# Performance work log

Hardware: AMD Instinct MI355X
Metric: run time of the kernel (lower is better)

The kernel has to match this reference:

```python
import jax, jax.numpy as jnp
import numpy as np

B, N, IN, OUT, H = 16, 1024, 512, 512, 4

def setup_inputs() -> dict:
    key = jax.random.key(0)
    ks = jax.random.split(key, 10)
    s = 0.03  # small init scale to keep tanh/sigmoid in sane range
    return {
        "h": jax.random.normal(ks[0], (B, N, IN), jnp.float32),
        "adj": jax.random.randint(ks[1], (B, N, N), 0, 2) > 0,
        "W": jax.random.normal(ks[2], (H, OUT, IN), jnp.float32) * s,   # per-head Linear weight [out,in]
        "bW": jax.random.normal(ks[3], (H, OUT), jnp.float32) * s,
        "attn": jax.random.normal(ks[4], (H, OUT, OUT), jnp.float32) * s,
        "A_w": jax.random.normal(ks[5], (OUT, OUT * H), jnp.float32) * s,
        "fc_w": jax.random.normal(ks[6], (OUT, IN), jnp.float32) * s,
        "g1_w": jax.random.normal(ks[7], (OUT, OUT), jnp.float32) * s,
        "g2_w": jax.random.normal(ks[8], (OUT, OUT), jnp.float32) * s,
        "gbias": jax.random.normal(ks[9], (OUT,), jnp.float32) * s,
    }

def reference(h, adj, W, bW, attn, A_w, fc_w, g1_w, g2_w, gbias):
    # Per-head projection: Wh[b,h,n,o] = h @ W_h^T + b_h  (dropout is identity at inference)
    Wh = jnp.einsum('bni,hoi->bhno', h, W) + bW[None, :, None, :]
    # Bilinear attention scores: Wh @ attn_h @ Wh^T, masked by adjacency, then tanh
    e = jnp.einsum('bhno,hop->bhnp', Wh, attn)          # [B,H,N,O]
    scores = jnp.einsum('bhnp,bhmp->bhnm', e, Wh)       # [B,H,N,N]
    A_mat = jnp.tanh(jnp.where(adj[:, None, :, :], scores, 0.0))
    # Aggregate neighbors and relu
    hp = jax.nn.relu(jnp.einsum('bhnm,bhmo->bhno', A_mat, Wh))  # [B,H,N,O]
    # Concat heads (relu of relu is identity), project with A
    cat = jnp.transpose(hp, (0, 2, 1, 3)).reshape(hp.shape[0], hp.shape[2], -1)  # [B,N,H*O]
    ha = cat @ A_w.T                                     # [B,N,O]
    hf = h @ fc_w.T                                      # [B,N,O]
    # Sigmoid-gated fusion of the two branches
    coeff = jax.nn.sigmoid(hf @ g1_w.T + ha @ g2_w.T + gbias)
    return hf * coeff + ha * (1.0 - coeff)
```

## Files before the change

### kernel.cpp

```cpp
#include <hip/hip_runtime.h>
#include <hip/hip_fp16.h>


typedef _Float16 h8 __attribute__((ext_vector_type(8)));
typedef _Float16 h4 __attribute__((ext_vector_type(4)));
typedef float f4 __attribute__((ext_vector_type(4)));

__device__ __forceinline__ void load_lds16(const void* g, void* l) {
  __builtin_amdgcn_global_load_lds(
      (const __attribute__((address_space(1))) unsigned int*)g,
      (__attribute__((address_space(3))) unsigned int*)l, 16, 0, 0);
}

struct GP {
  const _Float16* A; const _Float16* B; void* C; const float* bias;
  const unsigned long long* adjb; _Float16* aux;
  int K, ldA, ldB, ldC, z0, ntx, nty, nz;
  long sAz, sAb, sBz, sBh, sCz, sCb, sCh, sBiasH, sAuxZ;
};

__device__ __forceinline__ void stage_tiles(const _Float16* Ag, const _Float16* Bg,
                                            _Float16* As, _Float16* Bs,
                                            int ldA, int ldB, int wv, int rs, int cs) {
#pragma unroll
  for (int ps = 0; ps < 4; ++ps) {
    int c = ps * 4 + wv;
    int r = c * 8 + rs;
    int kb = (cs ^ (r & 7)) * 8;
    load_lds16(Ag + (long)r * ldA + kb, As + c * 512);
    load_lds16(Bg + (long)r * ldB + kb, Bs + c * 512);
  }
}

__device__ __forceinline__ void compute_tile(const _Float16* As, const _Float16* Bs,
                                             f4 acc[4][4], int wr, int wc, int l15, int lg) {
#pragma unroll
  for (int ks = 0; ks < 2; ++ks) {
    h8 av[4], bv[4];
    const int kby = ks * 64 + lg * 16;
#pragma unroll
    for (int m = 0; m < 4; ++m) {
      int row = wr * 64 + m * 16 + l15;
      av[m] = *(const h8*)((const char*)As + row * 128 + (kby ^ ((row & 7) << 4)));
    }
#pragma unroll
    for (int n = 0; n < 4; ++n) {
      int col = wc * 64 + n * 16 + l15;
      bv[n] = *(const h8*)((const char*)Bs + col * 128 + (kby ^ ((col & 7) << 4)));
    }
#pragma unroll
    for (int m = 0; m < 4; ++m)
#pragma unroll
      for (int n = 0; n < 4; ++n)
        acc[m][n] = __builtin_amdgcn_mfma_f32_16x16x32_f16(av[m], bv[n], acc[m][n], 0, 0, 0);
  }
}

template<int EPI>
__device__ __forceinline__ void gemm_core(GP p) {
  __shared__ __align__(16) char smem[32768];
  _Float16* Ash = (_Float16*)smem;
  _Float16* Bsh = (_Float16*)(smem + 16384);
  _Float16* Cld = (_Float16*)smem;

  const int tid = threadIdx.x;
  const int wv = tid >> 6;
  const int ln = tid & 63;
  const int l15 = ln & 15;
  const int lg = ln >> 4;
  const int wr = wv >> 1, wc = wv & 1;
  const int rs = ln >> 3;
  const int cs = ln & 7;

  const int bid = blockIdx.x;
  const int ntile = p.ntx * p.nty;
  int zl, tx, ty;
  if (p.nz > 1) {
    int xcd = bid & 7;
    int u = bid >> 3;
    zl = xcd + 8 * (u / ntile);
    int t = u % ntile;
    tx = t % p.ntx;
    ty = t / p.ntx;
  } else {
    int xcd = bid & 7;
    int u = bid >> 3;
    int t = xcd * (ntile >> 3) + u;
    zl = 0;
    tx = t % p.ntx;
    ty = t / p.ntx;
  }
  const int zg = p.z0 + zl;
  const int bg = zg >> 2, hg = zg & 3;
  const _Float16* A = p.A + p.sAz * zl + p.sAb * bg;
  const _Float16* Bm = p.B + p.sBz * zl + p.sBh * hg;
  const long m0 = (long)tx * 128;
  const long n0 = (long)ty * 128;
  const int nk = p.K >> 6;

  f4 acc[4][4];
#pragma unroll
  for (int i = 0; i < 4; ++i)
#pragma unroll
    for (int j = 0; j < 4; ++j) acc[i][j] = (f4)(0.0f);

  const _Float16* Ag = A + m0 * p.ldA;
  const _Float16* Bg = Bm + n0 * p.ldB;

  for (int kt = 0; kt < nk; ++kt) {
    stage_tiles(Ag + kt * 64, Bg + kt * 64, Ash, Bsh, p.ldA, p.ldB, wv, rs, cs);
    __syncthreads();
    compute_tile(Ash, Bsh, acc, wr, wc, l15, lg);
    __syncthreads();
  }

  const long coff = p.sCz * zl + p.sCb * bg + p.sCh * hg;
  const float* bias = p.bias ? (p.bias + p.sBiasH * hg) : nullptr;
#pragma unroll
  for (int m = 0; m < 4; ++m) {
#pragma unroll
    for (int j = 0; j < 4; ++j) {
      int lrow = wr * 64 + m * 16 + lg * 4 + j;
      long grow = m0 + lrow;
      int vx = (lrow & 12) << 2;
      unsigned long long w;
      if (EPI == 2)
        w = p.adjb[(long)bg * 16384 + grow * 16 + (n0 >> 6) + wc];
#pragma unroll
      for (int n = 0; n < 4; ++n) {
        int lcol = wc * 64 + n * 16 + l15;
        float v = acc[m][n][j];
        if (EPI == 5 || EPI == 6) v += bias[n0 + lcol];
        if (EPI == 2) {
          if ((w >> (n * 16 + l15)) & 1ull) {
            float ex = __expf(2.0f * v);
            v = 1.0f - 2.0f * __builtin_amdgcn_rcpf(ex + 1.0f);
          } else v = 0.0f;
        }
        if (EPI == 3) v = v > 0.0f ? v : 0.0f;
        if (EPI == 5) v = __builtin_amdgcn_rcpf(1.0f + __expf(-v));
        Cld[lrow * 128 + (lcol ^ vx)] = (_Float16)v;
      }
    }
  }
  __syncthreads();
  {
    _Float16* C = (_Float16*)p.C;
#pragma unroll
    for (int it = 0; it < 8; ++it) {
      int row = it * 16 + (tid >> 4);
      int col0 = (tid & 15) * 8;
      int vx = (row & 12) << 2;
      h8 o = *(const h8*)&Cld[row * 128 + (col0 ^ vx)];
      *(h8*)&C[coff + (m0 + row) * p.ldC + n0 + col0] = o;
    }
  }
  if (EPI == 6) {
    _Float16* X = p.aux + p.sAuxZ * zl;
#pragma unroll
    for (int pass = 0; pass < 8; ++pass) {
      int ol = pass * 16 + (tid >> 4);
      int ml = (tid & 15) * 8;
      h8 o;
#pragma unroll
      for (int j = 0; j < 8; ++j) {
        int mm = ml + j;
        o[j] = Cld[mm * 128 + (ol ^ ((mm & 12) << 2))];
      }
      *(h8*)&X[(n0 + ol) * 1024 + m0 + ml] = o;
    }
  }
}

#define GEMM_WRAP(name, epi) \
  __global__ __launch_bounds__(256) void name(GP p) { gemm_core<epi>(p); }
GEMM_WRAP(gemm_wh, 6)
GEMM_WRAP(gemm_e, 0)
GEMM_WRAP(gemm_amat, 2)
GEMM_WRAP(gemm_cat, 3)
GEMM_WRAP(gemm_hf, 0)
GEMM_WRAP(gemm_ha, 0)
GEMM_WRAP(gemm_gate, 5)

__global__ __launch_bounds__(256) void mix_kernel(const _Float16* gcat,
                                                  const _Float16* coeff, float* out) {
  const int stride = gridDim.x * 256;
  for (int g = blockIdx.x * 256 + threadIdx.x; g < 1048576; g += stride) {
    int r = g >> 6, c8 = (g & 63) << 3;
    h8 hf = *(const h8*)&gcat[(long)r * 1024 + c8];
    h8 ha = *(const h8*)&gcat[(long)r * 1024 + 512 + c8];
    h8 cf = *(const h8*)&coeff[(long)r * 512 + c8];
    float o[8];
#pragma unroll
    for (int j = 0; j < 8; ++j) {
      float c = (float)cf[j];
      o[j] = (float)hf[j] * c + (float)ha[j] * (1.0f - c);
    }
    float* op = &out[(long)r * 512 + c8];
    *(float4*)op = make_float4(o[0], o[1], o[2], o[3]);
    *(float4*)(op + 4) = make_float4(o[4], o[5], o[6], o[7]);
  }
}

__global__ void trans_attn(const float* attn, _Float16* attnT) {
  __shared__ _Float16 tl[64][65];
  const long hh = blockIdx.z;
  const float* I = attn + hh * 262144;
  _Float16* O = attnT + hh * 262144;
  const int r0 = blockIdx.x * 64, c0 = blockIdx.y * 64;
  for (int i = threadIdx.x; i < 4096; i += 256) {
    int r = i >> 6, c = i & 63;
    tl[c][r] = (_Float16)I[(long)(r0 + r) * 512 + c0 + c];
  }
  __syncthreads();
  for (int i = threadIdx.x; i < 4096; i += 256) {
    int c = i >> 6, r = i & 63;
    O[(long)(c0 + c) * 512 + r0 + r] = tl[c][r];
  }
}

__global__ void cvt_f16(const float* in, _Float16* out, int n4) {
  int i = blockIdx.x * 256 + threadIdx.x;
  if (i < n4) {
    float4 v = ((const float4*)in)[i];
    h4 o = {(_Float16)v.x, (_Float16)v.y, (_Float16)v.z, (_Float16)v.w};
    ((h4*)out)[i] = o;
  }
}

__global__ void build_gw(const float* g1, const float* g2, _Float16* gw) {
  int i = blockIdx.x * 256 + threadIdx.x;
  int o = i >> 10, k = i & 1023;
  float v = (k < 512) ? g1[o * 512 + k] : g2[o * 512 + (k - 512)];
  gw[i] = (_Float16)v;
}

__global__ void detect_fmt(const unsigned char* adj, int* flags) {
  __shared__ int sa, sb, sc;
  if (threadIdx.x == 0) { sa = 0; sb = 0; sc = 0; }
  __syncthreads();
  int a = 0, b = 0, c = 0;
  for (int i = threadIdx.x; i < 4096; i += 256) {
    if (adj[i]) {
      if (i & 3) a = 1;
      else c = 1;
      if ((i & 7) == 4) b = 1;
    }
  }
  if (a) sa = 1;
  if (b) sb = 1;
  if (c) sc = 1;
  __syncthreads();
  if (threadIdx.x == 0) {
    int fmt;
    if (sa) fmt = sc ? 1 : 3;
    else fmt = sb ? 0 : 2;
    flags[0] = fmt;
  }
}

__global__ void adj_bits(const void* adj, const int* flags, unsigned long long* adjb) {
  long i = (long)blockIdx.x * 256 + threadIdx.x;
  int fmt = flags[0];
  bool v;
  if (fmt == 1) v = ((const unsigned char*)adj)[i] != 0;
  else if (fmt == 3) v = ((const float*)adj)[i] != 0.0f;
  else if (fmt == 2) v = ((const long long*)adj)[i] != 0;
  else v = ((const int*)adj)[i] != 0;
  unsigned long long m = __ballot(v);
  if ((threadIdx.x & 63) == 0) adjb[i >> 6] = m;
}

extern "C" void kernel_launch(void* const* d_in, const int* in_sizes, int n_in,
                              void* d_out, int out_size, void* d_ws, size_t ws_size,
                              hipStream_t stream) {
  const float* h    = (const float*)d_in[0];
  const void*  adj  = d_in[1];
  const float* W    = (const float*)d_in[2];
  const float* bW   = (const float*)d_in[3];
  const float* attn = (const float*)d_in[4];
  const float* A_w  = (const float*)d_in[5];
  const float* fc_w = (const float*)d_in[6];
  const float* g1   = (const float*)d_in[7];
  const float* g2   = (const float*)d_in[8];
  const float* gbias= (const float*)d_in[9];
  float* out = (float*)d_out;
  char* ws = (char*)d_ws;
  (void)in_sizes; (void)n_in; (void)out_size;

  const size_t MB = 1ull << 20;
  const size_t fixedB = 92 * MB;
  int ZCv = 16;
  if (fixedB + 5ull * 64 * MB <= ws_size) ZCv = 64;
  else if (fixedB + 5ull * 32 * MB <= ws_size) ZCv = 32;
  const int nchunk = 64 / ZCv;

  size_t off = 0;
  auto alloc = [&](size_t sz) { size_t o = off; off += (sz + 255) & ~(size_t)255; return o; };
  const size_t oFlags = alloc(256);
  const size_t oH16   = alloc(16 * MB);
  const size_t oW16   = alloc(2 * MB);
  const size_t oAttnT = alloc(2 * MB);
  const size_t oAw16  = alloc(2 * MB);
  const size_t oFc16  = alloc(512 * 1024);
  const size_t oGw16  = alloc(1 * MB);
  const size_t oAdjb  = alloc(2 * MB);
  const size_t oCat   = alloc(64 * MB);
  const size_t oWhC   = alloc((size_t)ZCv * MB);
  const size_t oEC    = alloc((size_t)ZCv * MB);
  const size_t oWhTC  = alloc((size_t)ZCv * MB);
  const size_t oAmatC = alloc((size_t)ZCv * 2 * MB);
  const size_t oGcat  = oWhC;
  const size_t oCoeff = oAmatC;

  int* flags = (int*)(ws + oFlags);
  _Float16* h16   = (_Float16*)(ws + oH16);
  _Float16* W16   = (_Float16*)(ws + oW16);
  _Float16* attnT = (_Float16*)(ws + oAttnT);
  _Float16* Aw16  = (_Float16*)(ws + oAw16);
  _Float16* fc16  = (_Float16*)(ws + oFc16);
  _Float16* gw16  = (_Float16*)(ws + oGw16);
  unsigned long long* adjb = (unsigned long long*)(ws + oAdjb);
  _Float16* cat   = (_Float16*)(ws + oCat);
  _Float16* WhC   = (_Float16*)(ws + oWhC);
  _Float16* eC    = (_Float16*)(ws + oEC);
  _Float16* WhTC  = (_Float16*)(ws + oWhTC);
  _Float16* AmatC = (_Float16*)(ws + oAmatC);
  _Float16* gcat  = (_Float16*)(ws + oGcat);
  _Float16* coeff = (_Float16*)(ws + oCoeff);

  detect_fmt<<<1, 256, 0, stream>>>((const unsigned char*)adj, flags);
  adj_bits<<<65536, 256, 0, stream>>>(adj, flags, adjb);
  cvt_f16<<<8192, 256, 0, stream>>>(h, h16, 2097152);
  cvt_f16<<<1024, 256, 0, stream>>>(W, W16, 262144);
  cvt_f16<<<1024, 256, 0, stream>>>(A_w, Aw16, 262144);
  cvt_f16<<<256, 256, 0, stream>>>(fc_w, fc16, 65536);
  build_gw<<<2048, 256, 0, stream>>>(g1, g2, gw16);
  trans_attn<<<dim3(8, 8, 4), 256, 0, stream>>>(attn, attnT);

  for (int c = 0; c < nchunk; ++c) {
    const int z0 = c * ZCv;
    GP q;
    q = GP{};
    q.A = h16; q.B = W16; q.C = WhC; q.bias = bW; q.aux = WhTC;
    q.K = 512; q.ldA = 512; q.ldB = 512; q.ldC = 512; q.z0 = z0;
    q.ntx = 8; q.nty = 4; q.nz = ZCv;
    q.sAz = 0; q.sAb = 524288; q.sBz = 0; q.sBh = 262144;
    q.sCz = 524288; q.sCb = 0; q.sCh = 0; q.sBiasH = 512; q.sAuxZ = 524288;
    gemm_wh<<<32 * ZCv, 256, 0, stream>>>(q);
    q = GP{};
    q.A = WhC; q.B = attnT; q.C = eC;
    q.K = 512; q.ldA = 512; q.ldB = 512; q.ldC = 512; q.z0 = z0;
    q.ntx = 8; q.nty = 4; q.nz = ZCv;
    q.sAz = 524288; q.sBh = 262144; q.sCz = 524288;
    gemm_e<<<32 * ZCv, 256, 0, stream>>>(q);
    q = GP{};
    q.A = eC; q.B = WhC; q.C = AmatC; q.adjb = adjb;
    q.K = 512; q.ldA = 512; q.ldB = 512; q.ldC = 1024; q.z0 = z0;
    q.ntx = 8; q.nty = 8; q.nz = ZCv;
    q.sAz = 524288; q.sBz = 524288; q.sCz = 1048576;
    gemm_amat<<<64 * ZCv, 256, 0, stream>>>(q);
    q = GP{};
    q.A = AmatC; q.B = WhTC; q.C = cat;
    q.K = 1024; q.ldA = 1024; q.ldB = 1024; q.ldC = 2048; q.z0 = z0;
    q.sAz = 1048576; q.sBz = 524288;
    q.ntx = 8; q.nty = 4; q.nz = ZCv;
    q.sCz = 0; q.sCb = 2097152; q.sCh = 512;
    gemm_cat<<<32 * ZCv, 256, 0, stream>>>(q);
  }

  GP q;
  q = GP{};
  q.A = h16; q.B = fc16; q.C = gcat;
  q.K = 512; q.ldA = 512; q.ldB = 512; q.ldC = 1024; q.z0 = 0;
  q.ntx = 128; q.nty = 4; q.nz = 1;
  gemm_hf<<<512, 256, 0, stream>>>(q);
  q = GP{};
  q.A = cat; q.B = Aw16; q.C = gcat + 512;
  q.K = 2048; q.ldA = 2048; q.ldB = 2048; q.ldC = 1024; q.z0 = 0;
  q.ntx = 128; q.nty = 4; q.nz = 1;
  gemm_ha<<<512, 256, 0, stream>>>(q);
  q = GP{};
  q.A = gcat; q.B = gw16; q.C = coeff; q.bias = gbias;
  q.K = 1024; q.ldA = 1024; q.ldB = 1024; q.ldC = 512; q.z0 = 0;
  q.ntx = 128; q.nty = 4; q.nz = 1; q.sBiasH = 0;
  gemm_gate<<<512, 256, 0, stream>>>(q);
  mix_kernel<<<2048, 256, 0, stream>>>(gcat, coeff, out);
}
```

Measured before the change: 526.9 us.

## Enlarge GEMM tiles to 256x128 with 8x4 MFMA accumulators per wave

Changes the shared GEMM core from 128x128 to 256x128 output tiles. Each wave now computes 128x64, reusing its B fragments across twice as many MFMAs, and LDS grows to 48KB. The epilogue is split into two 128-row halves that reuse the LDS staging buffer. Grids are halved for every GEMM. This raises arithmetic intensity per LDS load but doubles accumulator registers and lowers occupancy and block count, so small per-chunk grids may underfill the GPU.

```diff
diff --git a/kernel.cpp b/kernel.cpp
--- a/kernel.cpp
+++ b/kernel.cpp
@@ -19,48 +19,52 @@
   long sAz, sAb, sBz, sBh, sCz, sCb, sCh, sBiasH, sAuxZ;
 };
 
-__device__ __forceinline__ void stage_tiles(const _Float16* Ag, const _Float16* Bg,
-                                            _Float16* As, _Float16* Bs,
-                                            int ldA, int ldB, int wv, int rs, int cs) {
-#pragma unroll
-  for (int ps = 0; ps < 4; ++ps) {
+__device__ __forceinline__ void stage_tiles2(const _Float16* Ag, const _Float16* Bg,
+                                             _Float16* As, _Float16* Bs,
+                                             int ldA, int ldB, int wv, int rs, int cs) {
+#pragma unroll
+  for (int ps = 0; ps < 12; ++ps) {
     int c = ps * 4 + wv;
-    int r = c * 8 + rs;
-    int kb = (cs ^ (r & 7)) * 8;
-    load_lds16(Ag + (long)r * ldA + kb, As + c * 512);
-    load_lds16(Bg + (long)r * ldB + kb, Bs + c * 512);
-  }
-}
-
-__device__ __forceinline__ void compute_tile(const _Float16* As, const _Float16* Bs,
-                                             f4 acc[4][4], int wr, int wc, int l15, int lg) {
+    if (c < 32) {
+      int r = c * 8 + rs;
+      int kb = (cs ^ (r & 7)) * 8;
+      load_lds16(Ag + (long)r * ldA + kb, As + c * 512);
+    } else {
+      int cb = c - 32;
+      int r = cb * 8 + rs;
+      int kb = (cs ^ (r & 7)) * 8;
+      load_lds16(Bg + (long)r * ldB + kb, Bs + cb * 512);
+    }
+  }
+}
+
+__device__ __forceinline__ void compute_tile2(const _Float16* As, const _Float16* Bs,
+                                              f4 acc[8][4], int wr, int wc, int l15, int lg) {
 #pragma unroll
   for (int ks = 0; ks < 2; ++ks) {
-    h8 av[4], bv[4];
     const int kby = ks * 64 + lg * 16;
-#pragma unroll
-    for (int m = 0; m < 4; ++m) {
-      int row = wr * 64 + m * 16 + l15;
-      av[m] = *(const h8*)((const char*)As + row * 128 + (kby ^ ((row & 7) << 4)));
-    }
+    h8 bv[4];
 #pragma unroll
     for (int n = 0; n < 4; ++n) {
       int col = wc * 64 + n * 16 + l15;
       bv[n] = *(const h8*)((const char*)Bs + col * 128 + (kby ^ ((col & 7) << 4)));
     }
 #pragma unroll
-    for (int m = 0; m < 4; ++m)
+    for (int m = 0; m < 8; ++m) {
+      int row = wr * 128 + m * 16 + l15;
+      h8 av = *(const h8*)((const char*)As + row * 128 + (kby ^ ((row & 7) << 4)));
 #pragma unroll
       for (int n = 0; n < 4; ++n)
-        acc[m][n] = __builtin_amdgcn_mfma_f32_16x16x32_f16(av[m], bv[n], acc[m][n], 0, 0, 0);
+        acc[m][n] = __builtin_amdgcn_mfma_f32_16x16x32_f16(av, bv[n], acc[m][n], 0, 0, 0);
+    }
   }
 }
 
 template<int EPI>
 __device__ __forceinline__ void gemm_core(GP p) {
-  __shared__ __align__(16) char smem[32768];
+  __shared__ __align__(16) char smem[49152];
   _Float16* Ash = (_Float16*)smem;
-  _Float16* Bsh = (_Float16*)(smem + 16384);
+  _Float16* Bsh = (_Float16*)(smem + 32768);
   _Float16* Cld = (_Float16*)smem;
 
   const int tid = threadIdx.x;
@@ -94,13 +98,13 @@
   const int bg = zg >> 2, hg = zg & 3;
   const _Float16* A = p.A + p.sAz * zl + p.sAb * bg;
   const _Float16* Bm = p.B + p.sBz * zl + p.sBh * hg;
-  const long m0 = (long)tx * 128;
+  const long m0 = (long)tx * 256;
   const long n0 = (long)ty * 128;
   const int nk = p.K >> 6;
 
-  f4 acc[4][4];
-#pragma unroll
-  for (int i = 0; i < 4; ++i)
+  f4 acc[8][4];
+#pragma unroll
+  for (int i = 0; i < 8; ++i)
 #pragma unroll
     for (int j = 0; j < 4; ++j) acc[i][j] = (f4)(0.0f);
 
@@ -108,66 +112,70 @@
   const _Float16* Bg = Bm + n0 * p.ldB;
 
   for (int kt = 0; kt < nk; ++kt) {
-    stage_tiles(Ag + kt * 64, Bg + kt * 64, Ash, Bsh, p.ldA, p.ldB, wv, rs, cs);
+    stage_tiles2(Ag + kt * 64, Bg + kt * 64, Ash, Bsh, p.ldA, p.ldB, wv, rs, cs);
     __syncthreads();
-    compute_tile(Ash, Bsh, acc, wr, wc, l15, lg);
+    compute_tile2(Ash, Bsh, acc, wr, wc, l15, lg);
     __syncthreads();
   }
 
   const long coff = p.sCz * zl + p.sCb * bg + p.sCh * hg;
   const float* bias = p.bias ? (p.bias + p.sBiasH * hg) : nullptr;
-#pragma unroll
-  for (int m = 0; m < 4; ++m) {
-#pragma unroll
-    for (int j = 0; j < 4; ++j) {
-      int lrow = wr * 64 + m * 16 + lg * 4 + j;
-      long grow = m0 + lrow;
-      int vx = (lrow & 12) << 2;
-      unsigned long long w;
-      if (EPI == 2)
-        w = p.adjb[(long)bg * 16384 + grow * 16 + (n0 >> 6) + wc];
-#pragma unroll
-      for (int n = 0; n < 4; ++n) {
-        int lcol = wc * 64 + n * 16 + l15;
-        float v = acc[m][n][j];
-        if (EPI == 5 || EPI == 6) v += bias[n0 + lcol];
-        if (EPI == 2) {
-          if ((w >> (n * 16 + l15)) & 1ull) {
-            float ex = __expf(2.0f * v);
-            v = 1.0f - 2.0f * __builtin_amdgcn_rcpf(ex + 1.0f);
-          } else v = 0.0f;
+  _Float16* C = (_Float16*)p.C;
+  _Float16* X = (EPI == 6) ? (p.aux + p.sAuxZ * zl) : nullptr;
+#pragma unroll
+  for (int hf2 = 0; hf2 < 2; ++hf2) {
+    __syncthreads();
+    if (wr == hf2) {
+#pragma unroll
+      for (int m = 0; m < 8; ++m) {
+#pragma unroll
+        for (int j = 0; j < 4; ++j) {
+          int lrow = m * 16 + lg * 4 + j;
+          long grow = m0 + hf2 * 128 + lrow;
+          int vx = (lrow & 12) << 2;
+          unsigned long long w;
+          if (EPI == 2)
+            w = p.adjb[(long)bg * 16384 + grow * 16 + (n0 >> 6) + wc];
+#pragma unroll
+          for (int n = 0; n < 4; ++n) {
+            int lcol = wc * 64 + n * 16 + l15;
+            float v = acc[m][n][j];
+            if (EPI == 5 || EPI == 6) v += bias[n0 + lcol];
+            if (EPI == 2) {
+              if ((w >> (n * 16 + l15)) & 1ull) {
+                float ex = __expf(2.0f * v);
+                v = 1.0f - 2.0f * __builtin_amdgcn_rcpf(ex + 1.0f);
+              } else v = 0.0f;
+            }
+            if (EPI == 3) v = v > 0.0f ? v : 0.0f;
+            if (EPI == 5) v = __builtin_amdgcn_rcpf(1.0f + __expf(-v));
+            Cld[lrow * 128 + (lcol ^ vx)] = (_Float16)v;
+          }
         }
-        if (EPI == 3) v = v > 0.0f ? v : 0.0f;
-        if (EPI == 5) v = __builtin_amdgcn_rcpf(1.0f + __expf(-v));
-        Cld[lrow * 128 + (lcol ^ vx)] = (_Float16)v;
       }
     }
-  }
-  __syncthreads();
-  {
-    _Float16* C = (_Float16*)p.C;
+    __syncthreads();
 #pragma unroll
     for (int it = 0; it < 8; ++it) {
       int row = it * 16 + (tid >> 4);
       int col0 = (tid & 15) * 8;
       int vx = (row & 12) << 2;
       h8 o = *(const h8*)&Cld[row * 128 + (col0 ^ vx)];
-      *(h8*)&C[coff + (m0 + row) * p.ldC + n0 + col0] = o;
-    }
-  }
-  if (EPI == 6) {
-    _Float16* X = p.aux + p.sAuxZ * zl;
-#pragma unroll
-    for (int pass = 0; pass < 8; ++pass) {
-      int ol = pass * 16 + (tid >> 4);
-      int ml = (tid & 15) * 8;
-      h8 o;
-#pragma unroll
-      for (int j = 0; j < 8; ++j) {
-        int mm = ml + j;
-        o[j] = Cld[mm * 128 + (ol ^ ((mm & 12) << 2))];
+      *(h8*)&C[coff + (m0 + hf2 * 128 + row) * p.ldC + n0 + col0] = o;
+    }
+    if (EPI == 6) {
+#pragma unroll
+      for (int pass = 0; pass < 8; ++pass) {
+        int ol = pass * 16 + (tid >> 4);
+        int ml = (tid & 15) * 8;
+        h8 o;
+#pragma unroll
+        for (int j = 0; j < 8; ++j) {
+          int mm = ml + j;
+          o[j] = Cld[mm * 128 + (ol ^ ((mm & 12) << 2))];
+        }
+        *(h8*)&X[(n0 + ol) * 1024 + m0 + hf2 * 128 + ml] = o;
       }
-      *(h8*)&X[(n0 + ol) * 1024 + m0 + ml] = o;
     }
   }
 }
@@ -344,46 +352,46 @@
     q = GP{};
     q.A = h16; q.B = W16; q.C = WhC; q.bias = bW; q.aux = WhTC;
     q.K = 512; q.ldA = 512; q.ldB = 512; q.ldC = 512; q.z0 = z0;
-    q.ntx = 8; q.nty = 4; q.nz = ZCv;
+    q.ntx = 4; q.nty = 4; q.nz = ZCv;
     q.sAz = 0; q.sAb = 524288; q.sBz = 0; q.sBh = 262144;
     q.sCz = 524288; q.sCb = 0; q.sCh = 0; q.sBiasH = 512; q.sAuxZ = 524288;
-    gemm_wh<<<32 * ZCv, 256, 0, stream>>>(q);
+    gemm_wh<<<16 * ZCv, 256, 0, stream>>>(q);
     q = GP{};
     q.A = WhC; q.B = attnT; q.C = eC;
     q.K = 512; q.ldA = 512; q.ldB = 512; q.ldC = 512; q.z0 = z0;
-    q.ntx = 8; q.nty = 4; q.nz = ZCv;
+    q.ntx = 4; q.nty = 4; q.nz = ZCv;
     q.sAz = 524288; q.sBh = 262144; q.sCz = 524288;
-    gemm_e<<<32 * ZCv, 256, 0, stream>>>(q);
+    gemm_e<<<16 * ZCv, 256, 0, stream>>>(q);
     q = GP{};
     q.A = eC; q.B = WhC; q.C = AmatC; q.adjb = adjb;
     q.K = 512; q.ldA = 512; q.ldB = 512; q.ldC = 1024; q.z0 = z0;
-    q.ntx = 8; q.nty = 8; q.nz = ZCv;
+    q.ntx = 4; q.nty = 8; q.nz = ZCv;
     q.sAz = 524288; q.sBz = 524288; q.sCz = 1048576;
-    gemm_amat<<<64 * ZCv, 256, 0, stream>>>(q);
+    gemm_amat<<<32 * ZCv, 256, 0, stream>>>(q);
     q = GP{};
     q.A = AmatC; q.B = WhTC; q.C = cat;
     q.K = 1024; q.ldA = 1024; q.ldB = 1024; q.ldC = 2048; q.z0 = z0;
     q.sAz = 1048576; q.sBz = 524288;
-    q.ntx = 8; q.nty = 4; q.nz = ZCv;
+    q.ntx = 4; q.nty = 4; q.nz = ZCv;
     q.sCz = 0; q.sCb = 2097152; q.sCh = 512;
-    gemm_cat<<<32 * ZCv, 256, 0, stream>>>(q);
+    gemm_cat<<<16 * ZCv, 256, 0, stream>>>(q);
   }
 
   GP q;
   q = GP{};
   q.A = h16; q.B = fc16; q.C = gcat;
   q.K = 512; q.ldA = 512; q.ldB = 512; q.ldC = 1024; q.z0 = 0;
-  q.ntx = 128; q.nty = 4; q.nz = 1;
-  gemm_hf<<<512, 256, 0, stream>>>(q);
+  q.ntx = 64; q.nty = 4; q.nz = 1;
+  gemm_hf<<<256, 256, 0, stream>>>(q);
   q = GP{};
   q.A = cat; q.B = Aw16; q.C = gcat + 512;
   q.K = 2048; q.ldA = 2048; q.ldB = 2048; q.ldC = 1024; q.z0 = 0;
-  q.ntx = 128; q.nty = 4; q.nz = 1;
-  gemm_ha<<<512, 256, 0, stream>>>(q);
+  q.ntx = 64; q.nty = 4; q.nz = 1;
+  gemm_ha<<<256, 256, 0, stream>>>(q);
   q = GP{};
   q.A = gcat; q.B = gw16; q.C = coeff; q.bias = gbias;
   q.K = 1024; q.ldA = 1024; q.ldB = 1024; q.ldC = 512; q.z0 = 0;
-  q.ntx = 128; q.nty = 4; q.nz = 1; q.sBiasH = 0;
-  gemm_gate<<<512, 256, 0, stream>>>(q);
+  q.ntx = 64; q.nty = 4; q.nz = 1; q.sBiasH = 0;
+  gemm_gate<<<256, 256, 0, stream>>>(q);
   mix_kernel<<<2048, 256, 0, stream>>>(gcat, coeff, out);
 }
```

Result: slower. 851.2 us (+61.6%).

## Enlarge GEMM block tile to 128x256 with 8 waves per block

Applied to the files above, without the earlier changes.

Every GEMM now uses 512-thread blocks that compute a 128x256 output tile instead of 128x128. The B tile and the shared-memory staging grow to match, and the epilogue writes its output in two 128-column halves through the same LDS buffer. The aim is to reuse each A tile across twice as many columns, cutting global loads and block count. In exchange it uses more LDS (48KB), halves the grid size, which can hurt occupancy and load balance on small launches, and adds syncs in the epilogue.

```diff
diff --git a/kernel.cpp b/kernel.cpp
--- a/kernel.cpp
+++ b/kernel.cpp
@@ -19,25 +19,31 @@
   long sAz, sAb, sBz, sBh, sCz, sCb, sCh, sBiasH, sAuxZ;
 };
 
-__device__ __forceinline__ void stage_tiles(const _Float16* Ag, const _Float16* Bg,
-                                            _Float16* As, _Float16* Bs,
-                                            int ldA, int ldB, int wv, int rs, int cs) {
-#pragma unroll
-  for (int ps = 0; ps < 4; ++ps) {
-    int c = ps * 4 + wv;
-    int r = c * 8 + rs;
-    int kb = (cs ^ (r & 7)) * 8;
-    load_lds16(Ag + (long)r * ldA + kb, As + c * 512);
-    load_lds16(Bg + (long)r * ldB + kb, Bs + c * 512);
-  }
-}
-
-__device__ __forceinline__ void compute_tile(const _Float16* As, const _Float16* Bs,
-                                             f4 acc[4][4], int wr, int wc, int l15, int lg) {
+__device__ __forceinline__ void stage_tiles3(const _Float16* Ag, const _Float16* Bg,
+                                             _Float16* As, _Float16* Bs,
+                                             int ldA, int ldB, int wv, int rs, int cs) {
+#pragma unroll
+  for (int ps = 0; ps < 6; ++ps) {
+    int c = ps * 8 + wv;
+    if (c < 16) {
+      int r = c * 8 + rs;
+      int kb = (cs ^ (r & 7)) * 8;
+      load_lds16(Ag + (long)r * ldA + kb, As + c * 512);
+    } else {
+      int cb = c - 16;
+      int r = cb * 8 + rs;
+      int kb = (cs ^ (r & 7)) * 8;
+      load_lds16(Bg + (long)r * ldB + kb, Bs + cb * 512);
+    }
+  }
+}
+
+__device__ __forceinline__ void compute_tile3(const _Float16* As, const _Float16* Bs,
+                                              f4 acc[4][4], int wr, int wc, int l15, int lg) {
 #pragma unroll
   for (int ks = 0; ks < 2; ++ks) {
+    const int kby = ks * 64 + lg * 16;
     h8 av[4], bv[4];
-    const int kby = ks * 64 + lg * 16;
 #pragma unroll
     for (int m = 0; m < 4; ++m) {
       int row = wr * 64 + m * 16 + l15;
@@ -58,7 +64,7 @@
 
 template<int EPI>
 __device__ __forceinline__ void gemm_core(GP p) {
-  __shared__ __align__(16) char smem[32768];
+  __shared__ __align__(16) char smem[49152];
   _Float16* Ash = (_Float16*)smem;
   _Float16* Bsh = (_Float16*)(smem + 16384);
   _Float16* Cld = (_Float16*)smem;
@@ -68,7 +74,7 @@
   const int ln = tid & 63;
   const int l15 = ln & 15;
   const int lg = ln >> 4;
-  const int wr = wv >> 1, wc = wv & 1;
+  const int wr = wv >> 2, wc = wv & 3;
   const int rs = ln >> 3;
   const int cs = ln & 7;
 
@@ -95,7 +101,7 @@
   const _Float16* A = p.A + p.sAz * zl + p.sAb * bg;
   const _Float16* Bm = p.B + p.sBz * zl + p.sBh * hg;
   const long m0 = (long)tx * 128;
-  const long n0 = (long)ty * 128;
+  const long n0 = (long)ty * 256;
   const int nk = p.K >> 6;
 
   f4 acc[4][4];
@@ -108,72 +114,77 @@
   const _Float16* Bg = Bm + n0 * p.ldB;
 
   for (int kt = 0; kt < nk; ++kt) {
-    stage_tiles(Ag + kt * 64, Bg + kt * 64, Ash, Bsh, p.ldA, p.ldB, wv, rs, cs);
+    stage_tiles3(Ag + kt * 64, Bg + kt * 64, Ash, Bsh, p.ldA, p.ldB, wv, rs, cs);
     __syncthreads();
-    compute_tile(Ash, Bsh, acc, wr, wc, l15, lg);
+    compute_tile3(Ash, Bsh, acc, wr, wc, l15, lg);
     __syncthreads();
   }
 
   const long coff = p.sCz * zl + p.sCb * bg + p.sCh * hg;
   const float* bias = p.bias ? (p.bias + p.sBiasH * hg) : nullptr;
-#pragma unroll
-  for (int m = 0; m < 4; ++m) {
-#pragma unroll
-    for (int j = 0; j < 4; ++j) {
-      int lrow = wr * 64 + m * 16 + lg * 4 + j;
-      long grow = m0 + lrow;
-      int vx = (lrow & 12) << 2;
-      unsigned long long w;
-      if (EPI == 2)
-        w = p.adjb[(long)bg * 16384 + grow * 16 + (n0 >> 6) + wc];
-#pragma unroll
-      for (int n = 0; n < 4; ++n) {
-        int lcol = wc * 64 + n * 16 + l15;
-        float v = acc[m][n][j];
-        if (EPI == 5 || EPI == 6) v += bias[n0 + lcol];
-        if (EPI == 2) {
-          if ((w >> (n * 16 + l15)) & 1ull) {
-            float ex = __expf(2.0f * v);
-            v = 1.0f - 2.0f * __builtin_amdgcn_rcpf(ex + 1.0f);
-          } else v = 0.0f;
+  _Float16* C = (_Float16*)p.C;
+  _Float16* X = (EPI == 6) ? (p.aux + p.sAuxZ * zl) : nullptr;
+#pragma unroll
+  for (int ch = 0; ch < 2; ++ch) {
+    __syncthreads();
+    if ((wc >> 1) == ch) {
+#pragma unroll
+      for (int m = 0; m < 4; ++m) {
+#pragma unroll
+        for (int j = 0; j < 4; ++j) {
+          int lrow = wr * 64 + m * 16 + lg * 4 + j;
+          long grow = m0 + lrow;
+          int vx = (lrow & 12) << 2;
+          unsigned long long w;
+          if (EPI == 2)
+            w = p.adjb[(long)bg * 16384 + grow * 16 + (n0 >> 6) + wc];
+#pragma unroll
+          for (int n = 0; n < 4; ++n) {
+            int lcol = (wc & 1) * 64 + n * 16 + l15;
+            float v = acc[m][n][j];
+            if (EPI == 5 || EPI == 6) v += bias[n0 + wc * 64 + n * 16 + l15];
+            if (EPI == 2) {
+              if ((w >> (n * 16 + l15)) & 1ull) {
+                float ex = __expf(2.0f * v);
+                v = 1.0f - 2.0f * __builtin_amdgcn_rcpf(ex + 1.0f);
+              } else v = 0.0f;
+            }
+            if (EPI == 3) v = v > 0.0f ? v : 0.0f;
+            if (EPI == 5) v = __builtin_amdgcn_rcpf(1.0f + __expf(-v));
+            Cld[lrow * 128 + (lcol ^ vx)] = (_Float16)v;
+          }
         }
-        if (EPI == 3) v = v > 0.0f ? v : 0.0f;
-        if (EPI == 5) v = __builtin_amdgcn_rcpf(1.0f + __expf(-v));
-        Cld[lrow * 128 + (lcol ^ vx)] = (_Float16)v;
       }
     }
-  }
-  __syncthreads();
-  {
-    _Float16* C = (_Float16*)p.C;
-#pragma unroll
-    for (int it = 0; it < 8; ++it) {
-      int row = it * 16 + (tid >> 4);
-      int col0 = (tid & 15) * 8;
-      int vx = (row & 12) << 2;
-      h8 o = *(const h8*)&Cld[row * 128 + (col0 ^ vx)];
-      *(h8*)&C[coff + (m0 + row) * p.ldC + n0 + col0] = o;
-    }
-  }
-  if (EPI == 6) {
-    _Float16* X = p.aux + p.sAuxZ * zl;
-#pragma unroll
-    for (int pass = 0; pass < 8; ++pass) {
-      int ol = pass * 16 + (tid >> 4);
-      int ml = (tid & 15) * 8;
-      h8 o;
-#pragma unroll
-      for (int j = 0; j < 8; ++j) {
-        int mm = ml + j;
-        o[j] = Cld[mm * 128 + (ol ^ ((mm & 12) << 2))];
+    __syncthreads();
+#pragma unroll
+    for (int it = 0; it < 4; ++it) {
+      int idx = it * 512 + tid;
+      int row = idx >> 4;
+      int col0 = (idx & 15) * 8;
+      h8 o = *(const h8*)&Cld[row * 128 + (col0 ^ ((row & 12) << 2))];
+      *(h8*)&C[coff + (m0 + row) * p.ldC + n0 + ch * 128 + col0] = o;
+    }
+    if (EPI == 6) {
+#pragma unroll
+      for (int it = 0; it < 4; ++it) {
+        int idx = it * 512 + tid;
+        int ol = idx >> 4;
+        int ml = (idx & 15) * 8;
+        h8 o;
+#pragma unroll
+        for (int j = 0; j < 8; ++j) {
+          int mm = ml + j;
+          o[j] = Cld[mm * 128 + (ol ^ ((mm & 12) << 2))];
+        }
+        *(h8*)&X[(n0 + ch * 128 + ol) * 1024 + m0 + ml] = o;
       }
-      *(h8*)&X[(n0 + ol) * 1024 + m0 + ml] = o;
     }
   }
 }
 
 #define GEMM_WRAP(name, epi) \
-  __global__ __launch_bounds__(256) void name(GP p) { gemm_core<epi>(p); }
+  __global__ __launch_bounds__(512) void name(GP p) { gemm_core<epi>(p); }
 GEMM_WRAP(gemm_wh, 6)
 GEMM_WRAP(gemm_e, 0)
 GEMM_WRAP(gemm_amat, 2)
@@ -344,46 +355,46 @@
     q = GP{};
     q.A = h16; q.B = W16; q.C = WhC; q.bias = bW; q.aux = WhTC;
     q.K = 512; q.ldA = 512; q.ldB = 512; q.ldC = 512; q.z0 = z0;
-    q.ntx = 8; q.nty = 4; q.nz = ZCv;
+    q.ntx = 8; q.nty = 2; q.nz = ZCv;
     q.sAz = 0; q.sAb = 524288; q.sBz = 0; q.sBh = 262144;
     q.sCz = 524288; q.sCb = 0; q.sCh = 0; q.sBiasH = 512; q.sAuxZ = 524288;
-    gemm_wh<<<32 * ZCv, 256, 0, stream>>>(q);
+    gemm_wh<<<16 * ZCv, 512, 0, stream>>>(q);
     q = GP{};
     q.A = WhC; q.B = attnT; q.C = eC;
     q.K = 512; q.ldA = 512; q.ldB = 512; q.ldC = 512; q.z0 = z0;
-    q.ntx = 8; q.nty = 4; q.nz = ZCv;
+    q.ntx = 8; q.nty = 2; q.nz = ZCv;
     q.sAz = 524288; q.sBh = 262144; q.sCz = 524288;
-    gemm_e<<<32 * ZCv, 256, 0, stream>>>(q);
+    gemm_e<<<16 * ZCv, 512, 0, stream>>>(q);
     q = GP{};
     q.A = eC; q.B = WhC; q.C = AmatC; q.adjb = adjb;
     q.K = 512; q.ldA = 512; q.ldB = 512; q.ldC = 1024; q.z0 = z0;
-    q.ntx = 8; q.nty = 8; q.nz = ZCv;
+    q.ntx = 8; q.nty = 4; q.nz = ZCv;
     q.sAz = 524288; q.sBz = 524288; q.sCz = 1048576;
-    gemm_amat<<<64 * ZCv, 256, 0, stream>>>(q);
+    gemm_amat<<<32 * ZCv, 512, 0, stream>>>(q);
     q = GP{};
     q.A = AmatC; q.B = WhTC; q.C = cat;
     q.K = 1024; q.ldA = 1024; q.ldB = 1024; q.ldC = 2048; q.z0 = z0;
     q.sAz = 1048576; q.sBz = 524288;
-    q.ntx = 8; q.nty = 4; q.nz = ZCv;
+    q.ntx = 8; q.nty = 2; q.nz = ZCv;
     q.sCz = 0; q.sCb = 2097152; q.sCh = 512;
-    gemm_cat<<<32 * ZCv, 256, 0, stream>>>(q);
+    gemm_cat<<<16 * ZCv, 512, 0, stream>>>(q);
   }
 
   GP q;
   q = GP{};
   q.A = h16; q.B = fc16; q.C = gcat;
   q.K = 512; q.ldA = 512; q.ldB = 512; q.ldC = 1024; q.z0 = 0;
-  q.ntx = 128; q.nty = 4; q.nz = 1;
-  gemm_hf<<<512, 256, 0, stream>>>(q);
+  q.ntx = 128; q.nty = 2; q.nz = 1;
+  gemm_hf<<<256, 512, 0, stream>>>(q);
   q = GP{};
   q.A = cat; q.B = Aw16; q.C = gcat + 512;
   q.K = 2048; q.ldA = 2048; q.ldB = 2048; q.ldC = 1024; q.z0 = 0;
-  q.ntx = 128; q.nty = 4; q.nz = 1;
-  gemm_ha<<<512, 256, 0, stream>>>(q);
+  q.ntx = 128; q.nty = 2; q.nz = 1;
+  gemm_ha<<<256, 512, 0, stream>>>(q);
   q = GP{};
   q.A = gcat; q.B = gw16; q.C = coeff; q.bias = gbias;
   q.K = 1024; q.ldA = 1024; q.ldB = 1024; q.ldC = 512; q.z0 = 0;
-  q.ntx = 128; q.nty = 4; q.nz = 1; q.sBiasH = 0;
-  gemm_gate<<<512, 256, 0, stream>>>(q);
+  q.ntx = 128; q.nty = 2; q.nz = 1; q.sBiasH = 0;
+  gemm_gate<<<256, 512, 0, stream>>>(q);
   mix_kernel<<<2048, 256, 0, stream>>>(gcat, coeff, out);
 }
```

Result: faster. 492.3 us (-6.6%).
